# Kernel tuning notes

Hardware: AMD Instinct MI355X
Metric: run time of the kernel (lower is better)

Reference implementation:

```python
import jax, jax.numpy as jnp
import numpy as np

B, N, M, E, C_IN, C_OUT = 4, 10000, 10000, 160000, 128, 128


def setup_inputs() -> dict:
    key = jax.random.key(0)
    k1, k2, k3, k4 = jax.random.split(key, 4)
    x = jax.random.normal(k1, (B, N, C_IN), dtype=jnp.float32)
    node_idx = jax.random.randint(k2, (B, 1, E), 0, N)
    hyedge_idx = jax.random.randint(k3, (B, 1, E), 0, M)
    H = jnp.concatenate([node_idx, hyedge_idx], axis=1).astype(jnp.int64)  # [B, 2, E]
    theta = jax.random.normal(k4, (C_IN, C_OUT), dtype=jnp.float32) * (1.0 / np.sqrt(C_IN))
    bias = jnp.zeros((C_OUT,), dtype=jnp.float32)
    return {"x": x, "H": H, "theta": theta, "bias": bias}


def _hyconv_single(xg, Hg):
    # xg: [N, D] (already x @ theta); Hg: [2, E]
    node_idx, hyedge_idx = Hg[0], Hg[1]
    ones = jnp.ones((E,), dtype=xg.dtype)
    # node -> hyperedge: mean over nodes incident to each hyperedge
    deg_e = jax.ops.segment_sum(ones, hyedge_idx, num_segments=M)  # [M]
    e_norm = (1.0 / deg_e)[hyedge_idx]  # [E]
    x_edge = jax.ops.segment_sum(xg[node_idx] * e_norm[:, None], hyedge_idx, num_segments=M)  # [M, D]
    # hyperedge -> node: mean over hyperedges incident to each node
    deg_n = jax.ops.segment_sum(ones, node_idx, num_segments=N)  # [N]
    n_norm = (1.0 / deg_n)[node_idx]  # [E]
    x_node = jax.ops.segment_sum(x_edge[hyedge_idx] * n_norm[:, None], node_idx, num_segments=N)  # [N, D]
    return x_node


def reference(x, H, theta, bias):
    xt = jnp.einsum('bnc,cd->bnd', x, theta)  # dense projection
    out = jax.vmap(_hyconv_single)(xt, H)  # [B, N, D]
    return out + bias
```

## Files before the change

### kernel.cpp

```cpp
#include <hip/hip_runtime.h>
#include <hip/hip_bf16.h>


#define BB 4
#define NN 10000
#define MM 10000
#define EE 160000
#define CC 128
#define BM (BB * MM)
#define BN (BB * NN)
#define NCOPY 8
#define CAPX 16

typedef unsigned short u16;
using bf16 = __hip_bfloat16;
using bf162 = __hip_bfloat162;
typedef unsigned u32x4 __attribute__((ext_vector_type(4)));
typedef float f32x4 __attribute__((ext_vector_type(4)));

__global__ __launch_bounds__(256) void build_gemm_k(const int* __restrict__ H,
                                                    int* __restrict__ ctr,
                                                    u16* __restrict__ srcA,
                                                    u16* __restrict__ srcB,
                                                    const float* __restrict__ x,
                                                    const float* __restrict__ theta,
                                                    bf16* __restrict__ xt) {
    __shared__ float sTh[64 * 128];
    __shared__ float sX[32 * 128];
    const int bi = blockIdx.x;

    if (bi % 3 != 0) {
        const int j = bi - bi / 3 - 1;
        const int g = j * 256 + threadIdx.x;
        if (g >= BB * EE) return;
        const int cp = bi & 7;
        const int b = g / EE, e = g - b * EE;
        const int nd = H[b * 2 * EE + e];
        const int he = H[b * 2 * EE + EE + e];
        const int bktA = b * MM + he;
        const int s = atomicAdd(&ctr[cp * (BM + BN) + bktA], 1);
        if (s < CAPX) srcA[((size_t)cp * BM + bktA) * CAPX + s] = (u16)nd;
        const int bktB = b * NN + nd;
        const int q = atomicAdd(&ctr[cp * (BM + BN) + BM + bktB], 1);
        if (q < CAPX) srcB[((size_t)cp * BN + bktB) * CAPX + q] = (u16)he;
        return;
    }

    const int tid = threadIdx.x;
    const int row0 = (bi / 3) * 32;
    {
        const float4* src = (const float4*)&x[row0 * 128];
        float4* dst = (float4*)sX;
#pragma unroll
        for (int i = 0; i < 4; ++i) dst[tid + 256 * i] = src[tid + 256 * i];
    }
    const int cg2 = (tid & 63) * 2;
    const int rg = tid >> 6;
    float ax[8], ay[8];
#pragma unroll
    for (int r = 0; r < 8; ++r) { ax[r] = 0.f; ay[r] = 0.f; }

    for (int half = 0; half < 2; ++half) {
        __syncthreads();
        {
            const float4* src = (const float4*)&theta[half * 64 * 128];
            float4* dst = (float4*)sTh;
#pragma unroll
            for (int i = 0; i < 8; ++i) dst[tid + 256 * i] = src[tid + 256 * i];
        }
        __syncthreads();
#pragma unroll
        for (int k4 = 0; k4 < 16; ++k4) {
            const int kk = 4 * k4;
            const float2 t0 = *(const float2*)&sTh[(kk + 0) * 128 + cg2];
            const float2 t1 = *(const float2*)&sTh[(kk + 1) * 128 + cg2];
            const float2 t2 = *(const float2*)&sTh[(kk + 2) * 128 + cg2];
            const float2 t3 = *(const float2*)&sTh[(kk + 3) * 128 + cg2];
#pragma unroll
            for (int r = 0; r < 8; ++r) {
                const float4 xv =
                    *(const float4*)&sX[(rg * 8 + r) * 128 + half * 64 + kk];
                ax[r] = fmaf(xv.x, t0.x, ax[r]); ay[r] = fmaf(xv.x, t0.y, ay[r]);
                ax[r] = fmaf(xv.y, t1.x, ax[r]); ay[r] = fmaf(xv.y, t1.y, ay[r]);
                ax[r] = fmaf(xv.z, t2.x, ax[r]); ay[r] = fmaf(xv.z, t2.y, ay[r]);
                ax[r] = fmaf(xv.w, t3.x, ax[r]); ay[r] = fmaf(xv.w, t3.y, ay[r]);
            }
        }
    }
#pragma unroll
    for (int r = 0; r < 8; ++r) {
        bf162 h;
        h.x = __float2bfloat16(ax[r]);
        h.y = __float2bfloat16(ay[r]);
        *(bf162*)&xt[(size_t)(row0 + rg * 8 + r) * 128 + cg2] = h;
    }
}

__device__ __forceinline__ float blo(unsigned w) { return __uint_as_float(w << 16); }
__device__ __forceinline__ float bhi(unsigned w) { return __uint_as_float(w & 0xffff0000u); }
__device__ __forceinline__ unsigned pk2(float a, float b) {
    bf162 h;
    h.x = __float2bfloat16(a);
    h.y = __float2bfloat16(b);
    return *(unsigned*)&h;
}

__device__ __forceinline__ void acc8(const uint4 pk, float* s) {
    s[0] += blo(pk.x); s[1] += bhi(pk.x);
    s[2] += blo(pk.y); s[3] += bhi(pk.y);
    s[4] += blo(pk.z); s[5] += bhi(pk.z);
    s[6] += blo(pk.w); s[7] += bhi(pk.w);
}

__device__ __forceinline__ int merge_lists(const int* __restrict__ ctr,
                                           const u16* __restrict__ src,
                                           int side_off, int Bx, int wid, int lane,
                                           u16* __restrict__ buf) {
    int cnt = 0;
    if (lane < NCOPY) {
        cnt = ctr[lane * (BM + BN) + side_off + wid];
        cnt = cnt > CAPX ? CAPX : cnt;
    }
    int pre = cnt;
#pragma unroll
    for (int d = 1; d < 8; d <<= 1) {
        int o = __shfl_up(pre, d, 64);
        if (lane >= d) pre += o;
    }
    const int base = pre - cnt;
    int total = __shfl(pre, 7, 64);
    total = total > 64 ? 64 : total;
    if (lane < NCOPY && cnt) {
        const u16* lst = src + ((size_t)lane * Bx + wid) * CAPX;
        const uint4 f0 = *(const uint4*)lst;
        const uint4 f1 = *(const uint4*)(lst + 8);
        const unsigned wd[8] = {f0.x, f0.y, f0.z, f0.w, f1.x, f1.y, f1.z, f1.w};
#pragma unroll
        for (int j = 0; j < CAPX; ++j) {
            const u16 v = (u16)((j & 1) ? (wd[j >> 1] >> 16) : (wd[j >> 1] & 0xffffu));
            const int p = base + j;
            if (j < cnt && p < 64) buf[p] = v;
        }
    }
    __syncthreads();
    return total;
}

__device__ __forceinline__ void swz_bucket(int blk, int tid, int& b, int& wid_local4) {
    const int xcd = blk & 7;
    b = xcd >> 1;
    const int jj = ((blk >> 3) << 1) | (xcd & 1);
    wid_local4 = jj * 4 + (tid >> 6);
}

__global__ __launch_bounds__(256) void phase1_pull(const bf16* __restrict__ xt,
                                                   const int* __restrict__ ctr,
                                                   const u16* __restrict__ srcA,
                                                   bf16* __restrict__ x_edge) {
    __shared__ __align__(16) u16 buf[4 * 64];
    int b, wl;
    swz_bucket(blockIdx.x, threadIdx.x, b, wl);
    const int wid = b * MM + wl;
    const int lane = threadIdx.x & 63;
    u16* wbuf = &buf[(threadIdx.x >> 6) * 64];
    const int total = merge_lists(ctr, srcA, 0, BM, wid, lane, wbuf);

    const bf16* base = xt + (size_t)b * NN * CC;
    const int g = lane >> 4;
    const int c16 = lane & 15;
    float s[8];
#pragma unroll
    for (int k = 0; k < 8; ++k) s[k] = 0.f;
    int i = 0;
    for (; i + 4 <= total; i += 4) {
        const int idx = wbuf[i + g];
        const uint4 pk = *(const uint4*)(base + (size_t)idx * CC + c16 * 8);
        acc8(pk, s);
    }
    if (i < total && g < total - i) {
        const int idx = wbuf[i + g];
        const uint4 pk = *(const uint4*)(base + (size_t)idx * CC + c16 * 8);
        acc8(pk, s);
    }
#pragma unroll
    for (int k = 0; k < 8; ++k) {
        s[k] += __shfl_xor(s[k], 16, 64);
        s[k] += __shfl_xor(s[k], 32, 64);
    }
    const float w = total ? 1.0f / (float)total : 0.f;
    if (g == 0) {
        u32x4 o;
        o.x = pk2(s[0] * w, s[1] * w);
        o.y = pk2(s[2] * w, s[3] * w);
        o.z = pk2(s[4] * w, s[5] * w);
        o.w = pk2(s[6] * w, s[7] * w);
        __builtin_nontemporal_store(o, (u32x4*)&x_edge[(size_t)wid * CC + c16 * 8]);
    }
}

__global__ __launch_bounds__(256) void phase2_pull(const bf16* __restrict__ x_edge,
                                                   const int* __restrict__ ctr,
                                                   const u16* __restrict__ srcB,
                                                   const float* __restrict__ bias,
                                                   float* __restrict__ out) {
    __shared__ __align__(16) u16 buf[4 * 64];
    int b, wl;
    swz_bucket(blockIdx.x, threadIdx.x, b, wl);
    const int wid = b * NN + wl;
    const int lane = threadIdx.x & 63;
    u16* wbuf = &buf[(threadIdx.x >> 6) * 64];
    const int total = merge_lists(ctr, srcB, BM, BN, wid, lane, wbuf);

    const bf16* base = x_edge + (size_t)b * MM * CC;
    const int g = lane >> 4;
    const int c16 = lane & 15;
    float s[8];
#pragma unroll
    for (int k = 0; k < 8; ++k) s[k] = 0.f;
    int i = 0;
    for (; i + 4 <= total; i += 4) {
        const int idx = wbuf[i + g];
        const uint4 pk = *(const uint4*)(base + (size_t)idx * CC + c16 * 8);
        acc8(pk, s);
    }
    if (i < total && g < total - i) {
        const int idx = wbuf[i + g];
        const uint4 pk = *(const uint4*)(base + (size_t)idx * CC + c16 * 8);
        acc8(pk, s);
    }
#pragma unroll
    for (int k = 0; k < 8; ++k) {
        s[k] += __shfl_xor(s[k], 16, 64);
        s[k] += __shfl_xor(s[k], 32, 64);
    }
    const float w = total ? 1.0f / (float)total : 0.f;
    if (g < 2) {
        const float4 bv = *(const float4*)&bias[c16 * 8 + g * 4];
        f32x4 o;
        if (g == 0) {
            o.x = s[0] * w + bv.x; o.y = s[1] * w + bv.y;
            o.z = s[2] * w + bv.z; o.w = s[3] * w + bv.w;
        } else {
            o.x = s[4] * w + bv.x; o.y = s[5] * w + bv.y;
            o.z = s[6] * w + bv.z; o.w = s[7] * w + bv.w;
        }
        __builtin_nontemporal_store(o, (f32x4*)&out[(size_t)wid * CC + c16 * 8 + g * 4]);
    }
}

extern "C" void kernel_launch(void* const* d_in, const int* in_sizes, int n_in,
                              void* d_out, int out_size, void* d_ws, size_t ws_size,
                              hipStream_t stream) {
    const float* x = (const float*)d_in[0];
    const int* H = (const int*)d_in[1];
    const float* theta = (const float*)d_in[2];
    const float* bias = (const float*)d_in[3];
    float* out = (float*)d_out;

    bf16* xt = (bf16*)d_ws;
    bf16* x_edge = xt + (size_t)BB * NN * CC;
    int* ctr = (int*)(x_edge + (size_t)BB * MM * CC);
    u16* srcA = (u16*)(ctr + NCOPY * (BM + BN));
    u16* srcB = srcA + (size_t)NCOPY * BM * CAPX;

    hipMemsetAsync(ctr, 0, (size_t)NCOPY * (BM + BN) * sizeof(int), stream);

    build_gemm_k<<<3750, 256, 0, stream>>>(H, ctr, srcA, srcB, x, theta, xt);
    phase1_pull<<<BM / 4, 256, 0, stream>>>(xt, ctr, srcA, x_edge);
    phase2_pull<<<BN / 4, 256, 0, stream>>>(x_edge, ctr, srcB, bias, out);
}
```

Before: 184.5 us.

## Merge phase2 bucket lists inside phase1 and process two edges per build thread

The build kernel now handles two edges per thread through int2 loads of H, and its block interleave changes so that GEMM and bucket-building blocks alternate in groups of eight. Phase1 merges both the hyperedge and the node bucket lists. It writes the merged node lists and their counts to a flat buffer, so phase2 only reads a contiguous 64-entry list instead of merging eight copies. This moves merge latency off phase2's critical path, at the cost of extra work and workspace traffic in phase1.

```diff
diff --git a/kernel.cpp b/kernel.cpp
--- a/kernel.cpp
+++ b/kernel.cpp
@@ -28,26 +28,38 @@
     __shared__ float sTh[64 * 128];
     __shared__ float sX[32 * 128];
     const int bi = blockIdx.x;
-
-    if (bi % 3 != 0) {
-        const int j = bi - bi / 3 - 1;
-        const int g = j * 256 + threadIdx.x;
-        if (g >= BB * EE) return;
+    const int idx = (bi >> 4) * 8 + (bi & 7);
+
+    if ((bi >> 3) & 1) {
+        if (idx >= 1250) return;
+        const int gidx = idx * 256 + threadIdx.x;
+        const int g0 = gidx * 2;
         const int cp = bi & 7;
-        const int b = g / EE, e = g - b * EE;
-        const int nd = H[b * 2 * EE + e];
-        const int he = H[b * 2 * EE + EE + e];
-        const int bktA = b * MM + he;
-        const int s = atomicAdd(&ctr[cp * (BM + BN) + bktA], 1);
-        if (s < CAPX) srcA[((size_t)cp * BM + bktA) * CAPX + s] = (u16)nd;
-        const int bktB = b * NN + nd;
-        const int q = atomicAdd(&ctr[cp * (BM + BN) + BM + bktB], 1);
-        if (q < CAPX) srcB[((size_t)cp * BN + bktB) * CAPX + q] = (u16)he;
+        const int b = g0 / EE, e = g0 - b * EE;
+        const int2 nd2 = *(const int2*)&H[b * 2 * EE + e];
+        const int2 he2 = *(const int2*)&H[b * 2 * EE + EE + e];
+        {
+            const int bktA = b * MM + he2.x;
+            const int s = atomicAdd(&ctr[cp * (BM + BN) + bktA], 1);
+            if (s < CAPX) srcA[((size_t)cp * BM + bktA) * CAPX + s] = (u16)nd2.x;
+            const int bktB = b * NN + nd2.x;
+            const int q = atomicAdd(&ctr[cp * (BM + BN) + BM + bktB], 1);
+            if (q < CAPX) srcB[((size_t)cp * BN + bktB) * CAPX + q] = (u16)he2.x;
+        }
+        {
+            const int bktA = b * MM + he2.y;
+            const int s = atomicAdd(&ctr[cp * (BM + BN) + bktA], 1);
+            if (s < CAPX) srcA[((size_t)cp * BM + bktA) * CAPX + s] = (u16)nd2.y;
+            const int bktB = b * NN + nd2.y;
+            const int q = atomicAdd(&ctr[cp * (BM + BN) + BM + bktB], 1);
+            if (q < CAPX) srcB[((size_t)cp * BN + bktB) * CAPX + q] = (u16)he2.y;
+        }
         return;
     }
 
+    if (idx >= 1250) return;
     const int tid = threadIdx.x;
-    const int row0 = (bi / 3) * 32;
+    const int row0 = idx * 32;
     {
         const float4* src = (const float4*)&x[row0 * 128];
         float4* dst = (float4*)sX;
@@ -112,40 +124,6 @@
     s[6] += blo(pk.w); s[7] += bhi(pk.w);
 }
 
-__device__ __forceinline__ int merge_lists(const int* __restrict__ ctr,
-                                           const u16* __restrict__ src,
-                                           int side_off, int Bx, int wid, int lane,
-                                           u16* __restrict__ buf) {
-    int cnt = 0;
-    if (lane < NCOPY) {
-        cnt = ctr[lane * (BM + BN) + side_off + wid];
-        cnt = cnt > CAPX ? CAPX : cnt;
-    }
-    int pre = cnt;
-#pragma unroll
-    for (int d = 1; d < 8; d <<= 1) {
-        int o = __shfl_up(pre, d, 64);
-        if (lane >= d) pre += o;
-    }
-    const int base = pre - cnt;
-    int total = __shfl(pre, 7, 64);
-    total = total > 64 ? 64 : total;
-    if (lane < NCOPY && cnt) {
-        const u16* lst = src + ((size_t)lane * Bx + wid) * CAPX;
-        const uint4 f0 = *(const uint4*)lst;
-        const uint4 f1 = *(const uint4*)(lst + 8);
-        const unsigned wd[8] = {f0.x, f0.y, f0.z, f0.w, f1.x, f1.y, f1.z, f1.w};
-#pragma unroll
-        for (int j = 0; j < CAPX; ++j) {
-            const u16 v = (u16)((j & 1) ? (wd[j >> 1] >> 16) : (wd[j >> 1] & 0xffffu));
-            const int p = base + j;
-            if (j < cnt && p < 64) buf[p] = v;
-        }
-    }
-    __syncthreads();
-    return total;
-}
-
 __device__ __forceinline__ void swz_bucket(int blk, int tid, int& b, int& wid_local4) {
     const int xcd = blk & 7;
     b = xcd >> 1;
@@ -156,14 +134,58 @@
 __global__ __launch_bounds__(256) void phase1_pull(const bf16* __restrict__ xt,
                                                    const int* __restrict__ ctr,
                                                    const u16* __restrict__ srcA,
+                                                   const u16* __restrict__ srcB,
+                                                   u16* __restrict__ flatB,
+                                                   int* __restrict__ cntB,
                                                    bf16* __restrict__ x_edge) {
-    __shared__ __align__(16) u16 buf[4 * 64];
+    __shared__ __align__(16) u16 bufA[4 * 64];
+    __shared__ __align__(16) u16 bufB[4 * 64];
     int b, wl;
     swz_bucket(blockIdx.x, threadIdx.x, b, wl);
-    const int wid = b * MM + wl;
+    const int widA = b * MM + wl;
+    const int widB = b * NN + wl;
     const int lane = threadIdx.x & 63;
-    u16* wbuf = &buf[(threadIdx.x >> 6) * 64];
-    const int total = merge_lists(ctr, srcA, 0, BM, wid, lane, wbuf);
+    const int w4 = threadIdx.x >> 6;
+    u16* wbufA = &bufA[w4 * 64];
+    u16* wbufB = &bufB[w4 * 64];
+
+    int cA = 0, cB = 0;
+    uint4 a0, a1, b0, b1;
+    if (lane < NCOPY) {
+        const u16* la = srcA + ((size_t)lane * BM + widA) * CAPX;
+        const u16* lb = srcB + ((size_t)lane * BN + widB) * CAPX;
+        a0 = *(const uint4*)la; a1 = *(const uint4*)(la + 8);
+        b0 = *(const uint4*)lb; b1 = *(const uint4*)(lb + 8);
+        cA = ctr[lane * (BM + BN) + widA];       cA = cA > CAPX ? CAPX : cA;
+        cB = ctr[lane * (BM + BN) + BM + widB];  cB = cB > CAPX ? CAPX : cB;
+    }
+    int pA = cA, pB = cB;
+#pragma unroll
+    for (int d = 1; d < 8; d <<= 1) {
+        const int oA = __shfl_up(pA, d, 64);
+        const int oB = __shfl_up(pB, d, 64);
+        if (lane >= d) { pA += oA; pB += oB; }
+    }
+    const int baseA = pA - cA, baseB = pB - cB;
+    int totA = __shfl(pA, 7, 64); totA = totA > 64 ? 64 : totA;
+    int totB = __shfl(pB, 7, 64); totB = totB > 64 ? 64 : totB;
+    if (lane < NCOPY) {
+        const unsigned wa[8] = {a0.x, a0.y, a0.z, a0.w, a1.x, a1.y, a1.z, a1.w};
+        const unsigned wb[8] = {b0.x, b0.y, b0.z, b0.w, b1.x, b1.y, b1.z, b1.w};
+#pragma unroll
+        for (int j = 0; j < CAPX; ++j) {
+            const u16 va = (u16)((j & 1) ? (wa[j >> 1] >> 16) : (wa[j >> 1] & 0xffffu));
+            const u16 vb = (u16)((j & 1) ? (wb[j >> 1] >> 16) : (wb[j >> 1] & 0xffffu));
+            const int pa = baseA + j, pb = baseB + j;
+            if (j < cA && pa < 64) wbufA[pa] = va;
+            if (j < cB && pb < 64) wbufB[pb] = vb;
+        }
+    }
+    __syncthreads();
+
+    if (lane < 8)
+        *(u32x4*)&flatB[(size_t)widB * 64 + lane * 8] = *(const u32x4*)&wbufB[lane * 8];
+    if (lane == 0) cntB[widB] = totB;
 
     const bf16* base = xt + (size_t)b * NN * CC;
     const int g = lane >> 4;
@@ -172,13 +194,13 @@
 #pragma unroll
     for (int k = 0; k < 8; ++k) s[k] = 0.f;
     int i = 0;
-    for (; i + 4 <= total; i += 4) {
-        const int idx = wbuf[i + g];
-        const uint4 pk = *(const uint4*)(base + (size_t)idx * CC + c16 * 8);
-        acc8(pk, s);
-    }
-    if (i < total && g < total - i) {
-        const int idx = wbuf[i + g];
+    for (; i + 4 <= totA; i += 4) {
+        const int idx = wbufA[i + g];
+        const uint4 pk = *(const uint4*)(base + (size_t)idx * CC + c16 * 8);
+        acc8(pk, s);
+    }
+    if (i < totA && g < totA - i) {
+        const int idx = wbufA[i + g];
         const uint4 pk = *(const uint4*)(base + (size_t)idx * CC + c16 * 8);
         acc8(pk, s);
     }
@@ -187,20 +209,20 @@
         s[k] += __shfl_xor(s[k], 16, 64);
         s[k] += __shfl_xor(s[k], 32, 64);
     }
-    const float w = total ? 1.0f / (float)total : 0.f;
+    const float w = totA ? 1.0f / (float)totA : 0.f;
     if (g == 0) {
         u32x4 o;
         o.x = pk2(s[0] * w, s[1] * w);
         o.y = pk2(s[2] * w, s[3] * w);
         o.z = pk2(s[4] * w, s[5] * w);
         o.w = pk2(s[6] * w, s[7] * w);
-        __builtin_nontemporal_store(o, (u32x4*)&x_edge[(size_t)wid * CC + c16 * 8]);
+        __builtin_nontemporal_store(o, (u32x4*)&x_edge[(size_t)widA * CC + c16 * 8]);
     }
 }
 
 __global__ __launch_bounds__(256) void phase2_pull(const bf16* __restrict__ x_edge,
-                                                   const int* __restrict__ ctr,
-                                                   const u16* __restrict__ srcB,
+                                                   const u16* __restrict__ flatB,
+                                                   const int* __restrict__ cntB,
                                                    const float* __restrict__ bias,
                                                    float* __restrict__ out) {
     __shared__ __align__(16) u16 buf[4 * 64];
@@ -209,7 +231,11 @@
     const int wid = b * NN + wl;
     const int lane = threadIdx.x & 63;
     u16* wbuf = &buf[(threadIdx.x >> 6) * 64];
-    const int total = merge_lists(ctr, srcB, BM, BN, wid, lane, wbuf);
+    const int t0 = cntB[wid];
+    if (lane < 8)
+        *(u32x4*)&wbuf[lane * 8] = *(const u32x4*)&flatB[(size_t)wid * 64 + lane * 8];
+    __syncthreads();
+    const int total = t0 > 64 ? 64 : t0;
 
     const bf16* base = x_edge + (size_t)b * MM * CC;
     const int g = lane >> 4;
@@ -262,10 +288,12 @@
     int* ctr = (int*)(x_edge + (size_t)BB * MM * CC);
     u16* srcA = (u16*)(ctr + NCOPY * (BM + BN));
     u16* srcB = srcA + (size_t)NCOPY * BM * CAPX;
+    u16* flatB = srcB + (size_t)NCOPY * BN * CAPX;
+    int* cntB = (int*)(flatB + (size_t)BN * 64);
 
     hipMemsetAsync(ctr, 0, (size_t)NCOPY * (BM + BN) * sizeof(int), stream);
 
-    build_gemm_k<<<3750, 256, 0, stream>>>(H, ctr, srcA, srcB, x, theta, xt);
-    phase1_pull<<<BM / 4, 256, 0, stream>>>(xt, ctr, srcA, x_edge);
-    phase2_pull<<<BN / 4, 256, 0, stream>>>(x_edge, ctr, srcB, bias, out);
-}
+    build_gemm_k<<<2512, 256, 0, stream>>>(H, ctr, srcA, srcB, x, theta, xt);
+    phase1_pull<<<BM / 4, 256, 0, stream>>>(xt, ctr, srcA, srcB, flatB, cntB, x_edge);
+    phase2_pull<<<BN / 4, 256, 0, stream>>>(x_edge, flatB, cntB, bias, out);
+}
```

New measurement: 179.7 us. 2.6% less time.

## Replace 8-way split counters with per-bucket 256-byte records holding count and list

Applied to the files above, without the earlier changes.

Swaps the eight replicated counter arrays and separate capped source lists for one 256-byte record per bucket. Each record holds two halves, each with an inline atomic counter and up to 62 indices, and each half is fed by a fixed half of the edges. Edge blocks are interleaved with GEMM blocks in an XCD-aware order and handle two edges per thread. The pull kernels now read the whole record with one vector load instead of running a prefix-sum merge over eight lists. The intent is fewer scattered counter and list accesses and simpler merging, at the cost of more atomic contention per counter and a larger memset.

```diff
diff --git a/kernel.cpp b/kernel.cpp
--- a/kernel.cpp
+++ b/kernel.cpp
@@ -9,8 +9,7 @@
 #define CC 128
 #define BM (BB * MM)
 #define BN (BB * NN)
-#define NCOPY 8
-#define CAPX 16
+#define CAPR 62
 
 typedef unsigned short u16;
 using bf16 = __hip_bfloat16;
@@ -19,37 +18,44 @@
 typedef float f32x4 __attribute__((ext_vector_type(4)));
 
 __global__ __launch_bounds__(256) void build_gemm_k(const int* __restrict__ H,
-                                                    int* __restrict__ ctr,
-                                                    u16* __restrict__ srcA,
-                                                    u16* __restrict__ srcB,
+                                                    u16* __restrict__ recA,
+                                                    u16* __restrict__ recB,
                                                     const float* __restrict__ x,
                                                     const float* __restrict__ theta,
                                                     bf16* __restrict__ xt) {
     __shared__ float sTh[64 * 128];
     __shared__ float sX[32 * 128];
     const int bi = blockIdx.x;
-
-    if (bi % 3 != 0) {
-        const int j = bi - bi / 3 - 1;
-        const int g = j * 256 + threadIdx.x;
-        if (g >= BB * EE) return;
-        const int cp = bi & 7;
-        const int b = g / EE, e = g - b * EE;
-        const int nd = H[b * 2 * EE + e];
-        const int he = H[b * 2 * EE + EE + e];
-        const int bktA = b * MM + he;
-        const int s = atomicAdd(&ctr[cp * (BM + BN) + bktA], 1);
-        if (s < CAPX) srcA[((size_t)cp * BM + bktA) * CAPX + s] = (u16)nd;
-        const int bktB = b * NN + nd;
-        const int q = atomicAdd(&ctr[cp * (BM + BN) + BM + bktB], 1);
-        if (q < CAPX) srcB[((size_t)cp * BN + bktB) * CAPX + q] = (u16)he;
+    const int idx = (bi >> 4) * 8 + (bi & 7);
+
+    if ((bi >> 3) & 1) {
+        const int xcd = idx & 7;
+        const int kk = idx >> 3;
+        const int b = xcd >> 1, m = xcd & 1;
+        const int ee = (kk * 256 + (int)threadIdx.x) * 2;
+        if (ee >= 80000) return;
+        const int e = m * 80000 + ee;
+        const int2 nd2 = *(const int2*)&H[b * 2 * EE + e];
+        const int2 he2 = *(const int2*)&H[b * 2 * EE + EE + e];
+        const int nd[2] = {nd2.x, nd2.y};
+        const int he[2] = {he2.x, he2.y};
+#pragma unroll
+        for (int t = 0; t < 2; ++t) {
+            int* ca = (int*)(recA + ((size_t)(b * MM + he[t]) * 128 + m * 64));
+            const int s = atomicAdd(ca, 1);
+            if (s < CAPR) ((u16*)ca)[2 + s] = (u16)nd[t];
+            int* cb = (int*)(recB + ((size_t)(b * NN + nd[t]) * 128 + m * 64));
+            const int q = atomicAdd(cb, 1);
+            if (q < CAPR) ((u16*)cb)[2 + q] = (u16)he[t];
+        }
         return;
     }
 
+    if (idx >= 1250) return;
     const int tid = threadIdx.x;
-    const int row0 = (bi / 3) * 32;
+    const int row0 = idx * 32;
     {
-        const float4* src = (const float4*)&x[row0 * 128];
+        const float4* src = (const float4*)&x[(size_t)row0 * 128];
         float4* dst = (float4*)sX;
 #pragma unroll
         for (int i = 0; i < 4; ++i) dst[tid + 256 * i] = src[tid + 256 * i];
@@ -112,40 +118,6 @@
     s[6] += blo(pk.w); s[7] += bhi(pk.w);
 }
 
-__device__ __forceinline__ int merge_lists(const int* __restrict__ ctr,
-                                           const u16* __restrict__ src,
-                                           int side_off, int Bx, int wid, int lane,
-                                           u16* __restrict__ buf) {
-    int cnt = 0;
-    if (lane < NCOPY) {
-        cnt = ctr[lane * (BM + BN) + side_off + wid];
-        cnt = cnt > CAPX ? CAPX : cnt;
-    }
-    int pre = cnt;
-#pragma unroll
-    for (int d = 1; d < 8; d <<= 1) {
-        int o = __shfl_up(pre, d, 64);
-        if (lane >= d) pre += o;
-    }
-    const int base = pre - cnt;
-    int total = __shfl(pre, 7, 64);
-    total = total > 64 ? 64 : total;
-    if (lane < NCOPY && cnt) {
-        const u16* lst = src + ((size_t)lane * Bx + wid) * CAPX;
-        const uint4 f0 = *(const uint4*)lst;
-        const uint4 f1 = *(const uint4*)(lst + 8);
-        const unsigned wd[8] = {f0.x, f0.y, f0.z, f0.w, f1.x, f1.y, f1.z, f1.w};
-#pragma unroll
-        for (int j = 0; j < CAPX; ++j) {
-            const u16 v = (u16)((j & 1) ? (wd[j >> 1] >> 16) : (wd[j >> 1] & 0xffffu));
-            const int p = base + j;
-            if (j < cnt && p < 64) buf[p] = v;
-        }
-    }
-    __syncthreads();
-    return total;
-}
-
 __device__ __forceinline__ void swz_bucket(int blk, int tid, int& b, int& wid_local4) {
     const int xcd = blk & 7;
     b = xcd >> 1;
@@ -153,17 +125,31 @@
     wid_local4 = jj * 4 + (tid >> 6);
 }
 
+__device__ __forceinline__ void load_rec(const u16* __restrict__ rec, int wid,
+                                         int lane, u16* __restrict__ wbuf,
+                                         int& c0, int& c1) {
+    if (lane < 16)
+        *(u32x4*)&wbuf[lane * 8] =
+            *(const u32x4*)(rec + (size_t)wid * 128 + lane * 8);
+    __syncthreads();
+    c0 = *(const int*)&wbuf[0];
+    c1 = *(const int*)&wbuf[64];
+    c0 = c0 > CAPR ? CAPR : c0;
+    c1 = c1 > CAPR ? CAPR : c1;
+}
+
 __global__ __launch_bounds__(256) void phase1_pull(const bf16* __restrict__ xt,
-                                                   const int* __restrict__ ctr,
-                                                   const u16* __restrict__ srcA,
+                                                   const u16* __restrict__ recA,
                                                    bf16* __restrict__ x_edge) {
-    __shared__ __align__(16) u16 buf[4 * 64];
+    __shared__ __align__(16) u16 buf[4 * 128];
     int b, wl;
     swz_bucket(blockIdx.x, threadIdx.x, b, wl);
     const int wid = b * MM + wl;
     const int lane = threadIdx.x & 63;
-    u16* wbuf = &buf[(threadIdx.x >> 6) * 64];
-    const int total = merge_lists(ctr, srcA, 0, BM, wid, lane, wbuf);
+    u16* wbuf = &buf[(threadIdx.x >> 6) * 128];
+    int c0, c1;
+    load_rec(recA, wid, lane, wbuf, c0, c1);
+    const int total = c0 + c1;
 
     const bf16* base = xt + (size_t)b * NN * CC;
     const int g = lane >> 4;
@@ -173,12 +159,16 @@
     for (int k = 0; k < 8; ++k) s[k] = 0.f;
     int i = 0;
     for (; i + 4 <= total; i += 4) {
-        const int idx = wbuf[i + g];
+        const int t = i + g;
+        const int l = t < c0 ? (t + 2) : (t + 66 - c0);
+        const int idx = wbuf[l];
         const uint4 pk = *(const uint4*)(base + (size_t)idx * CC + c16 * 8);
         acc8(pk, s);
     }
     if (i < total && g < total - i) {
-        const int idx = wbuf[i + g];
+        const int t = i + g;
+        const int l = t < c0 ? (t + 2) : (t + 66 - c0);
+        const int idx = wbuf[l];
         const uint4 pk = *(const uint4*)(base + (size_t)idx * CC + c16 * 8);
         acc8(pk, s);
     }
@@ -194,22 +184,23 @@
         o.y = pk2(s[2] * w, s[3] * w);
         o.z = pk2(s[4] * w, s[5] * w);
         o.w = pk2(s[6] * w, s[7] * w);
-        __builtin_nontemporal_store(o, (u32x4*)&x_edge[(size_t)wid * CC + c16 * 8]);
+        *(u32x4*)&x_edge[(size_t)wid * CC + c16 * 8] = o;
     }
 }
 
 __global__ __launch_bounds__(256) void phase2_pull(const bf16* __restrict__ x_edge,
-                                                   const int* __restrict__ ctr,
-                                                   const u16* __restrict__ srcB,
+                                                   const u16* __restrict__ recB,
                                                    const float* __restrict__ bias,
                                                    float* __restrict__ out) {
-    __shared__ __align__(16) u16 buf[4 * 64];
+    __shared__ __align__(16) u16 buf[4 * 128];
     int b, wl;
     swz_bucket(blockIdx.x, threadIdx.x, b, wl);
     const int wid = b * NN + wl;
     const int lane = threadIdx.x & 63;
-    u16* wbuf = &buf[(threadIdx.x >> 6) * 64];
-    const int total = merge_lists(ctr, srcB, BM, BN, wid, lane, wbuf);
+    u16* wbuf = &buf[(threadIdx.x >> 6) * 128];
+    int c0, c1;
+    load_rec(recB, wid, lane, wbuf, c0, c1);
+    const int total = c0 + c1;
 
     const bf16* base = x_edge + (size_t)b * MM * CC;
     const int g = lane >> 4;
@@ -219,12 +210,16 @@
     for (int k = 0; k < 8; ++k) s[k] = 0.f;
     int i = 0;
     for (; i + 4 <= total; i += 4) {
-        const int idx = wbuf[i + g];
+        const int t = i + g;
+        const int l = t < c0 ? (t + 2) : (t + 66 - c0);
+        const int idx = wbuf[l];
         const uint4 pk = *(const uint4*)(base + (size_t)idx * CC + c16 * 8);
         acc8(pk, s);
     }
     if (i < total && g < total - i) {
-        const int idx = wbuf[i + g];
+        const int t = i + g;
+        const int l = t < c0 ? (t + 2) : (t + 66 - c0);
+        const int idx = wbuf[l];
         const uint4 pk = *(const uint4*)(base + (size_t)idx * CC + c16 * 8);
         acc8(pk, s);
     }
@@ -259,13 +254,12 @@
 
     bf16* xt = (bf16*)d_ws;
     bf16* x_edge = xt + (size_t)BB * NN * CC;
-    int* ctr = (int*)(x_edge + (size_t)BB * MM * CC);
-    u16* srcA = (u16*)(ctr + NCOPY * (BM + BN));
-    u16* srcB = srcA + (size_t)NCOPY * BM * CAPX;
-
-    hipMemsetAsync(ctr, 0, (size_t)NCOPY * (BM + BN) * sizeof(int), stream);
-
-    build_gemm_k<<<3750, 256, 0, stream>>>(H, ctr, srcA, srcB, x, theta, xt);
-    phase1_pull<<<BM / 4, 256, 0, stream>>>(xt, ctr, srcA, x_edge);
-    phase2_pull<<<BN / 4, 256, 0, stream>>>(x_edge, ctr, srcB, bias, out);
-}
+    u16* recA = (u16*)(x_edge + (size_t)BB * MM * CC);
+    u16* recB = recA + (size_t)BM * 128;
+
+    hipMemsetAsync(recA, 0, (size_t)(BM + BN) * 256, stream);
+
+    build_gemm_k<<<2512, 256, 0, stream>>>(H, recA, recB, x, theta, xt);
+    phase1_pull<<<BM / 4, 256, 0, stream>>>(xt, recA, x_edge);
+    phase2_pull<<<BN / 4, 256, 0, stream>>>(x_edge, recB, bias, out);
+}
```

New measurement: 220.9 us. 19.8% more time.
